# Optimization experiments

Hardware: AMD Instinct MI355X
Metric: run time of the kernel (lower is better)

## Reference

```python
import jax, jax.numpy as jnp
import numpy as np

DIM = 256
B, W_IN, H_IN = 8, 96, 96


def setup_inputs() -> dict:
    key = jax.random.key(0)
    k1, k2, k3 = jax.random.split(key, 3)
    x = jax.random.normal(k1, (B, W_IN, H_IN, DIM), dtype=jnp.float32)
    # Conv2d(dim, 3*dim, kernel_size=1): weight (3C, C) (1x1 spatial dropped), bias (3C,)
    w_qkv = jax.random.normal(k2, (3 * DIM, DIM), dtype=jnp.float32) * (1.0 / np.sqrt(DIM))
    b_qkv = jax.random.normal(k3, (3 * DIM,), dtype=jnp.float32) * 0.01
    return {"x": x, "w_qkv": w_qkv, "b_qkv": b_qkv}


def reference(x, w_qkv, b_qkv):
    # x: (B, W, H, C) -> transpose(3,1) -> (B, C, H, W)
    xt = jnp.transpose(x, (0, 3, 2, 1))
    # 1x1 conv == channel GEMM
    qvk = jnp.einsum('bchw,oc->bohw', xt, w_qkv) + b_qkv[None, :, None, None]
    q, k, v = jnp.split(qvk, 3, axis=1)  # each (B, C, H, W)
    Bn, C, H, W = q.shape

    q_t = jnp.transpose(q, (0, 2, 1, 3))            # (B, H, C, W)
    qk = q_t.reshape(Bn, H * C, W)                   # (B, H*C, W)
    qf = q_t.reshape(Bn, H, C * W)                   # (B, H, C*W)
    kq = jnp.transpose(k, (0, 1, 3, 2)).reshape(Bn, C * W, H)  # (B, C*W, H)
    ms = jax.nn.softmax(jnp.matmul(qf, kq), axis=-1)  # (B, H, H) attention over H

    kf = jnp.transpose(k, (0, 3, 2, 1)).reshape(Bn, W, H * C)  # (B, W, H*C)
    ma = jax.nn.softmax(jnp.matmul(kf, qk), axis=-1)  # (B, W, W) attention over W

    vq = jnp.transpose(v, (0, 2, 1, 3)).reshape(Bn, H, C * W)  # (B, H, C*W)
    vk = jnp.transpose(v, (0, 3, 2, 1)).reshape(Bn, W, H * C)  # (B, W, H*C)

    ms = jnp.matmul(ms, vq).reshape(Bn, H, C, W)     # view(B, H, C, W)
    ms = jnp.transpose(ms, (0, 2, 1, 3))             # (B, C, H, W)
    ma = jnp.matmul(ma, vk).reshape(Bn, W, H, C)     # view(B, W, H, C)
    ma = jnp.transpose(ma, (0, 3, 2, 1))             # (B, C, H, W)

    # final transpose(3,1): (B, C, H, W) -> (B, W, H, C)
    return jnp.transpose(ms + ma, (0, 3, 2, 1))
```

## Files before the change

kernel.cpp:

```cpp
#include <hip/hip_runtime.h>
#include <math.h>

#define SQ 96
#define CQ 256
#define HWQ 9216
#define PIXQ 73728

typedef __attribute__((ext_vector_type(8))) __bf16 bf16x8;
typedef __attribute__((ext_vector_type(4))) float f32x4;

union FragU { uint4 u; bf16x8 b; };

__device__ inline uint32_t bf16_rne_u(float f) {
  uint32_t u = __float_as_uint(f);
  return (u + 0x7FFFu + ((u >> 16) & 1u)) >> 16;
}
__device__ inline uint32_t pack_split(float f) {
  uint32_t hi = bf16_rne_u(f);
  float rem = f - __uint_as_float(hi << 16);
  uint32_t lo = __float_as_uint(rem) >> 16;
  return hi | (lo << 16);
}

__device__ inline const uint32_t* swzc(const uint32_t* base, int row, int colb) {
  return base + row * 32 + ((colb ^ ((row & 7) << 4)) >> 2);
}

__device__ inline void lds_dma16(const void* g, void* l) {
  __builtin_amdgcn_global_load_lds(
      (const __attribute__((address_space(1))) uint32_t*)g,
      (__attribute__((address_space(3))) uint32_t*)l, 16, 0, 0);
}

__device__ inline void pack8_store(float4 va, float4 vb_, int m, int kc,
                                   int k8, uint32_t* __restrict__ dst) {
  uint32_t p0 = pack_split(va.x), p1 = pack_split(va.y);
  uint32_t p2 = pack_split(va.z), p3 = pack_split(va.w);
  uint32_t p4 = pack_split(vb_.x), p5 = pack_split(vb_.y);
  uint32_t p6 = pack_split(vb_.z), p7 = pack_split(vb_.w);
  uint32_t h[4], l[4];
  h[0] = (p0 & 0xFFFFu) | (p1 << 16);
  h[1] = (p2 & 0xFFFFu) | (p3 << 16);
  h[2] = (p4 & 0xFFFFu) | (p5 << 16);
  h[3] = (p6 & 0xFFFFu) | (p7 << 16);
  l[0] = (p0 >> 16) | (p1 & 0xFFFF0000u);
  l[1] = (p2 >> 16) | (p3 & 0xFFFF0000u);
  l[2] = (p4 >> 16) | (p5 & 0xFFFF0000u);
  l[3] = (p6 >> 16) | (p7 & 0xFFFF0000u);
  int swz = (m & 7) << 4;
  uint32_t* rowp = dst + ((size_t)m * 8 + kc) * 32;
  *(uint4*)(rowp + (((k8 * 16) ^ swz) >> 2)) = *(uint4*)h;
  *(uint4*)(rowp + (((64 + k8 * 16) ^ swz) >> 2)) = *(uint4*)l;
}

__global__ __launch_bounds__(256) void prep_b_kernel(
    const float* __restrict__ w, uint32_t* __restrict__ Bps) {
  __shared__ float grow[256];
  const int blk = blockIdx.x;
  if (blk < 256) {
    const int cp = threadIdx.x;
    float acc = 0.0f;
#pragma unroll 4
    for (int o = 0; o < 256; ++o)
      acc += w[o * 256 + blk] * w[(256 + o) * 256 + cp];
    grow[cp] = acc;
    __syncthreads();
    if (threadIdx.x < 32) {
      int rem = threadIdx.x * 8;
      float4 va = *(const float4*)(grow + rem);
      float4 vb_ = *(const float4*)(grow + rem + 4);
      pack8_store(va, vb_, blk, rem >> 5, (rem & 31) >> 3, Bps);
    }
  } else {
    int r = (blk - 256) * 8 + (threadIdx.x >> 5);
    int rem = (threadIdx.x & 31) * 8;
    const float* s = w + (size_t)(512 + r) * 256 + rem;
    float4 va = *(const float4*)s;
    float4 vb_ = *(const float4*)(s + 4);
    pack8_store(va, vb_, 256 + r, rem >> 5, (rem & 31) >> 3, Bps);
  }
}

__global__ __launch_bounds__(256) void prep_vec_kernel(
    const float* __restrict__ w, const float* __restrict__ bias,
    float* __restrict__ tvec, float* __restrict__ svec) {
  const int c = threadIdx.x;
  if (blockIdx.x == 0) {
    float t = 0.0f;
#pragma unroll 4
    for (int o = 0; o < 256; ++o) t += bias[o] * w[(256 + o) * 256 + c];
    tvec[c] = t;
  } else {
    float s = 0.0f;
#pragma unroll 4
    for (int o = 0; o < 256; ++o) s += bias[256 + o] * w[o * 256 + c];
    svec[c] = s;
  }
}

__global__ __launch_bounds__(256) void split_x_kernel(
    const float* __restrict__ x, const float* __restrict__ tvec,
    const float* __restrict__ svec, uint32_t* __restrict__ xps,
    float* __restrict__ dtp, float* __restrict__ dsp) {
  int rec = blockIdx.x * 256 + threadIdx.x;
  int m = rec >> 3;
  int kc = rec & 7;
  const float* s = x + (size_t)m * 256 + kc * 32;
  const float* tv = tvec + kc * 32;
  const float* sv = svec + kc * 32;
  float dt = 0.0f, ds = 0.0f;
#pragma unroll
  for (int g = 0; g < 4; ++g) {
    float4 va = *(const float4*)(s + g * 8);
    float4 vb_ = *(const float4*)(s + g * 8 + 4);
    pack8_store(va, vb_, m, kc, g, xps);
    const float* tg = tv + g * 8;
    const float* sg = sv + g * 8;
    dt += va.x * tg[0] + va.y * tg[1] + va.z * tg[2] + va.w * tg[3]
        + vb_.x * tg[4] + vb_.y * tg[5] + vb_.z * tg[6] + vb_.w * tg[7];
    ds += va.x * sg[0] + va.y * sg[1] + va.z * sg[2] + va.w * sg[3]
        + vb_.x * sg[4] + vb_.y * sg[5] + vb_.z * sg[6] + vb_.w * sg[7];
  }
#pragma unroll
  for (int off = 1; off < 8; off <<= 1) {
    dt += __shfl_xor(dt, off);
    ds += __shfl_xor(ds, off);
  }
  if ((rec & 7) == 0) {
    dtp[m] = dt;
    dsp[m] = ds;
  }
}

__global__ __launch_bounds__(256) void reduce_ag_kernel(
    const float* __restrict__ dtp, const float* __restrict__ dsp,
    float* __restrict__ alpha, float* __restrict__ gamma) {
  const int b = blockIdx.x;
  const int t = threadIdx.x;
  if (t < 96) {
    float a = 0.0f;
#pragma unroll 4
    for (int wi = 0; wi < 96; ++wi) a += dtp[b * HWQ + wi * SQ + t];
    alpha[b * SQ + t] = a;
  } else if (t >= 128 && t < 224) {
    int wi = t - 128;
    float g = 0.0f;
#pragma unroll 4
    for (int hh = 0; hh < 96; ++hh) g += dsp[b * HWQ + wi * SQ + hh];
    gamma[b * SQ + wi] = g;
  }
}

__global__ __launch_bounds__(256) void qkv_gemm_mfma(
    const uint32_t* __restrict__ xps, const uint32_t* __restrict__ Bps,
    const float* __restrict__ bias, ushort* __restrict__ yps,
    ushort* __restrict__ vb) {
  __shared__ uint32_t Apk[128 * 32];
  __shared__ uint32_t Bpk[128 * 32];
  const int tid = threadIdx.x;
  const int lane = tid & 63;
  const int wid = tid >> 6;
  const int wm = wid >> 1, wn = wid & 1;
  const int lr = lane & 15, quad = lane >> 4;
  const int lin = (blockIdx.x & 7) * 288 + (blockIdx.x >> 3);
  const int m0 = (lin >> 2) * 128, n0 = (lin & 3) * 128;
  const int srow = tid >> 3;
  const int scol = (tid & 7) * 4;

  const uint32_t* aP = xps + (size_t)(m0 + srow) * 256 + scol;
  const uint32_t* bP = Bps + (size_t)(n0 + srow) * 256 + scol;

  f32x4 acc[4][4] = {};

  for (int kc = 0; kc < 8; ++kc) {
#pragma unroll
    for (int j = 0; j < 4; ++j) {
      lds_dma16(aP + j * 8192 + kc * 32, &Apk[j * 1024 + tid * 4]);
      lds_dma16(bP + j * 8192 + kc * 32, &Bpk[j * 1024 + tid * 4]);
    }
    __syncthreads();

    FragU ah[4], al[4], bh[4], bl[4];
#pragma unroll
    for (int t = 0; t < 4; ++t) {
      const int ra = wm * 64 + t * 16 + lr;
      ah[t].u = *(const uint4*)swzc(Apk, ra, quad * 16);
      al[t].u = *(const uint4*)swzc(Apk, ra, 64 + quad * 16);
      const int rb = wn * 64 + t * 16 + lr;
      bh[t].u = *(const uint4*)swzc(Bpk, rb, quad * 16);
      bl[t].u = *(const uint4*)swzc(Bpk, rb, 64 + quad * 16);
    }
#pragma unroll
    for (int i = 0; i < 4; ++i)
#pragma unroll
      for (int j = 0; j < 4; ++j) {
        acc[i][j] = __builtin_amdgcn_mfma_f32_16x16x32_bf16(al[i].b, bh[j].b, acc[i][j], 0, 0, 0);
        acc[i][j] = __builtin_amdgcn_mfma_f32_16x16x32_bf16(ah[i].b, bl[j].b, acc[i][j], 0, 0, 0);
        acc[i][j] = __builtin_amdgcn_mfma_f32_16x16x32_bf16(ah[i].b, bh[j].b, acc[i][j], 0, 0, 0);
      }
    __syncthreads();
  }

  if (n0 < 256) {
#pragma unroll
    for (int i = 0; i < 4; ++i) {
      const int growb = m0 + wm * 64 + i * 16 + quad * 4;
#pragma unroll
      for (int r = 0; r < 4; ++r) {
        int p = growb + r;
        size_t b16 = (size_t)p * 512;
        int sw = (p & 7) << 4;
#pragma unroll
        for (int j = 0; j < 4; ++j) {
          int o = n0 + wn * 64 + j * 16 + lr;
          int ci = o & 31, kc = o >> 5;
          uint32_t ps = pack_split(acc[i][j][r]);
          size_t rb = b16 + (size_t)kc * 64;
          yps[rb + (((ci * 2) ^ sw) >> 1)] = (ushort)ps;
          yps[rb + (((64 + ci * 2) ^ sw) >> 1)] = (ushort)(ps >> 16);
        }
      }
    }
  } else {
#pragma unroll
    for (int i = 0; i < 4; ++i) {
      const int growb = m0 + wm * 64 + i * 16 + quad * 4;
#pragma unroll
      for (int r = 0; r < 4; ++r) {
        int p = growb + r;
        int b = p / HWQ;
        int rem = p - b * HWQ;
        int ww = rem / SQ;
        int hh = rem - ww * SQ;
        size_t opix = (size_t)b * HWQ + (size_t)hh * SQ + ww;
#pragma unroll
        for (int j = 0; j < 4; ++j) {
          int o = n0 + wn * 64 + j * 16 + lr;
          float val = acc[i][j][r] + bias[256 + o];
          vb[opix * 256 + (o - 256)] = (ushort)bf16_rne_u(val);
        }
      }
    }
  }
}

__global__ __launch_bounds__(256) void attn_scores_mfma(
    const ushort* __restrict__ xf, const ushort* __restrict__ yf,
    float* __restrict__ Sp) {
  __shared__ uint32_t Xpk[96 * 32];
  __shared__ uint32_t Ypk[96 * 32];
  const int tid = threadIdx.x;
  const int lane = tid & 63;
  const int wid = tid >> 6;
  const int wm = wid >> 1, wn = wid & 1;
  const int lr = lane & 15, quad = lane >> 4;
  const int chunk = blockIdx.x;
  const int b = blockIdx.y;
  const int which = blockIdx.z;
  const ushort* Xf = which ? yf : xf;
  const ushort* Yf = which ? xf : yf;
  const int srow = tid >> 3;
  const int byteoff = (tid & 7) * 16;

  f32x4 acc[3][3] = {};

  for (int it = 0; it < 24; ++it) {
    int kout = chunk * 3 + (it >> 3);
    int kc = it & 7;
#pragma unroll
    for (int j = 0; j < 3; ++j) {
      int row = j * 32 + srow;
      int pm = which ? (row * SQ + kout) : (kout * SQ + row);
      int pix = b * HWQ + pm;
      int nom = byteoff ^ (((row & 7) ^ (pix & 7)) << 4);
      size_t off = ((size_t)pix * 8 + kc) * 64 + (nom >> 1);
      lds_dma16(Xf + off, &Xpk[j * 1024 + tid * 4]);
      lds_dma16(Yf + off, &Ypk[j * 1024 + tid * 4]);
    }
    __syncthreads();

    FragU xh[3], xl[3], yh[3], yl[3];
#pragma unroll
    for (int t = 0; t < 3; ++t) {
      const int rx = wm * 48 + t * 16 + lr;
      xh[t].u = *(const uint4*)swzc(Xpk, rx, quad * 16);
      xl[t].u = *(const uint4*)swzc(Xpk, rx, 64 + quad * 16);
      const int ry = wn * 48 + t * 16 + lr;
      yh[t].u = *(const uint4*)swzc(Ypk, ry, quad * 16);
      yl[t].u = *(const uint4*)swzc(Ypk, ry, 64 + quad * 16);
    }
#pragma unroll
    for (int i = 0; i < 3; ++i)
#pragma unroll
      for (int j = 0; j < 3; ++j) {
        acc[i][j] = __builtin_amdgcn_mfma_f32_16x16x32_bf16(xl[i].b, yh[j].b, acc[i][j], 0, 0, 0);
        acc[i][j] = __builtin_amdgcn_mfma_f32_16x16x32_bf16(xh[i].b, yl[j].b, acc[i][j], 0, 0, 0);
        acc[i][j] = __builtin_amdgcn_mfma_f32_16x16x32_bf16(xh[i].b, yh[j].b, acc[i][j], 0, 0, 0);
      }
    __syncthreads();
  }
  float* S = Sp + ((size_t)(which * 8 + b) * 32 + chunk) * (size_t)HWQ;
#pragma unroll
  for (int i = 0; i < 3; ++i)
#pragma unroll
    for (int r = 0; r < 4; ++r)
#pragma unroll
      for (int j = 0; j < 3; ++j) {
        int row = wm * 48 + i * 16 + quad * 4 + r;
        int col = wn * 48 + j * 16 + lr;
        S[(size_t)row * SQ + col] = acc[i][j][r];
      }
}

__global__ __launch_bounds__(256) void softmax_p(
    const float* __restrict__ Sp, const float* __restrict__ alpha,
    const float* __restrict__ gamma, ushort* __restrict__ Pms,
    ushort* __restrict__ Pma) {
  const int tid = threadIdx.x;
  const int lane = tid & 63;
  const int row = blockIdx.x * 4 + (tid >> 6);
  const int wsel = row >= 768;
  const int rr = row - wsel * 768;
  const int b = rr / SQ;
  const int hr = rr - b * SQ;
  const float* base = Sp + ((size_t)(wsel * 8 + b) * 32) * (size_t)HWQ
                      + (size_t)hr * SQ;
  float v0 = 0.0f, s1 = 0.0f;
#pragma unroll 4
  for (int ch = 0; ch < 32; ++ch) {
    const float* p = base + (size_t)ch * HWQ;
    v0 += p[lane];
    if (lane < 32) s1 += p[64 + lane];
  }
  const float* corr = (wsel ? gamma : alpha) + b * SQ;
  v0 += corr[lane];
  ushort* q = wsel ? (Pma + (size_t)rr * SQ) : (Pms + (size_t)rr * SQ);
  float v1 = (lane < 32) ? (s1 + corr[64 + lane]) : -3.0e38f;
  float m = fmaxf(v0, v1);
#pragma unroll
  for (int off = 32; off > 0; off >>= 1) m = fmaxf(m, __shfl_xor(m, off));
  float e0 = __expf(v0 - m);
  float e1 = (lane < 32) ? __expf(v1 - m) : 0.0f;
  float s = e0 + e1;
#pragma unroll
  for (int off = 32; off > 0; off >>= 1) s += __shfl_xor(s, off);
  float inv = 1.0f / s;
  q[lane] = (ushort)bf16_rne_u(e0 * inv);
  if (lane < 32) q[64 + lane] = (ushort)bf16_rne_u(e1 * inv);
}

__global__ __launch_bounds__(256) void attn_apply_mfma(
    const ushort* __restrict__ vb, const ushort* __restrict__ P,
    float* __restrict__ out, const int which) {
  __shared__ ushort Vt[256 * 40];
  const int tid = threadIdx.x;
  const int lane = tid & 63;
  const int wid = tid >> 6;
  const int wm = wid >> 1, wn = wid & 1;
  const int lr = lane & 15, quad = lane >> 4;
  const int xi = blockIdx.x;
  const int b = blockIdx.y;

  f32x4 acc[3][8] = {};

  for (int k0 = 0; k0 < 96; k0 += 32) {
#pragma unroll
    for (int j = 0; j < 8; ++j) {
      int bi = j * 256 + tid;
      int c2 = bi & 127;
      int k2 = bi >> 7;
      int k = k0 + k2 * 2;
      int c = c2 * 2;
      size_t r0, r1;
      if (which == 0) {
        r0 = ((size_t)b * HWQ + (size_t)k * SQ + xi) * CQ + c;
        r1 = r0 + (size_t)SQ * CQ;
      } else {
        r0 = ((size_t)b * HWQ + (size_t)xi * SQ + k) * CQ + c;
        r1 = r0 + CQ;
      }
      uint32_t a0 = *(const uint32_t*)(vb + r0);
      uint32_t a1 = *(const uint32_t*)(vb + r1);
      uint32_t w0 = (a0 & 0xFFFFu) | (a1 << 16);
      uint32_t w1 = (a0 >> 16) | (a1 & 0xFFFF0000u);
      *(uint32_t*)&Vt[c * 40 + k2 * 2] = w0;
      *(uint32_t*)&Vt[(c + 1) * 40 + k2 * 2] = w1;
    }
    __syncthreads();
    FragU a[3];
#pragma unroll
    for (int t = 0; t < 3; ++t) {
      int row = wm * 48 + t * 16 + lr;
      const ushort* ps = P + ((size_t)b * SQ + row) * SQ + k0 + quad * 8;
      a[t].u = *(const uint4*)ps;
    }
#pragma unroll
    for (int j = 0; j < 8; ++j) {
      int cb = wn * 128 + j * 16 + lr;
      FragU bf;
      bf.u = *(const uint4*)&Vt[cb * 40 + quad * 8];
#pragma unroll
      for (int i = 0; i < 3; ++i)
        acc[i][j] = __builtin_amdgcn_mfma_f32_16x16x32_bf16(a[i].b, bf.b, acc[i][j], 0, 0, 0);
    }
    __syncthreads();
  }

#pragma unroll
  for (int i = 0; i < 3; ++i) {
#pragma unroll
    for (int r = 0; r < 4; ++r) {
      int mrow = wm * 48 + i * 16 + quad * 4 + r;
      size_t obase;
      if (which == 0) obase = (((size_t)b * SQ + xi) * SQ + mrow) * CQ;
      else            obase = (((size_t)b * SQ + mrow) * SQ + xi) * CQ;
#pragma unroll
      for (int j = 0; j < 8; ++j) {
        int c = wn * 128 + j * 16 + lr;
        if (which == 0) out[obase + c] = acc[i][j][r];
        else            out[obase + c] += acc[i][j][r];
      }
    }
  }
}

extern "C" void kernel_launch(void* const* d_in, const int* in_sizes, int n_in,
                              void* d_out, int out_size, void* d_ws,
                              size_t ws_size, hipStream_t stream) {
  const float* x = (const float*)d_in[0];
  const float* w = (const float*)d_in[1];
  const float* bias = (const float*)d_in[2];
  float* out = (float*)d_out;

  ushort* yps = (ushort*)d_ws;
  ushort* vb  = yps + (size_t)PIXQ * 512;
  ushort* Pms = vb + (size_t)PIXQ * 256;
  ushort* Pma = Pms + PIXQ;
  float*  Sp  = (float*)(Pma + PIXQ);
  uint32_t* Bps = (uint32_t*)(Sp + (size_t)2 * 8 * 32 * HWQ);
  float* tvec = (float*)(Bps + 512 * 256);
  float* svec = tvec + 256;
  float* alpha = svec + 256;
  float* gamma = alpha + 768;
  float* dtp = gamma + 768;
  float* dsp = dtp + PIXQ;

  uint32_t* xps = (uint32_t*)d_out;

  prep_b_kernel<<<dim3(288), 256, 0, stream>>>(w, Bps);
  prep_vec_kernel<<<dim3(2), 256, 0, stream>>>(w, bias, tvec, svec);
  split_x_kernel<<<dim3(2304), 256, 0, stream>>>(x, tvec, svec, xps, dtp, dsp);
  reduce_ag_kernel<<<dim3(8), 256, 0, stream>>>(dtp, dsp, alpha, gamma);
  qkv_gemm_mfma<<<dim3(2304), 256, 0, stream>>>(xps, Bps, bias, yps, vb);
  attn_scores_mfma<<<dim3(32, 8, 2), 256, 0, stream>>>((const ushort*)xps, yps, Sp);
  softmax_p<<<dim3(384), 256, 0, stream>>>(Sp, alpha, gamma, Pms, Pma);
  attn_apply_mfma<<<dim3(96, 8), 256, 0, stream>>>(vb, Pms, out, 0);
  attn_apply_mfma<<<dim3(96, 8), 256, 0, stream>>>(vb, Pma, out, 1);
}
```

Before: 436.5 us.

## Store split-bf16 operands unswizzled and swizzle on load; split attn_apply channels

Packed hi/lo bf16 operands are now written to global memory in linear order, and the XOR swizzle is applied on the load side (per-thread source column in the GEMM, LDS DMA offsets in the scores kernel). This makes the packing stores contiguous, and split_x now writes whole records as grouped vector stores. attn_apply_mfma is split across two channel halves via blockIdx.z, halving its accumulator registers and LDS and doubling the grid. A XOR slot swizzle is added to its transposed V tile in LDS to reduce bank conflicts. The cost is extra index arithmetic, and the added P-matrix reloads across the two channel blocks.

```diff
diff --git a/kernel.cpp b/kernel.cpp
--- a/kernel.cpp
+++ b/kernel.cpp
@@ -32,25 +32,26 @@
       (__attribute__((address_space(3))) uint32_t*)l, 16, 0, 0);
 }
 
-__device__ inline void pack8_store(float4 va, float4 vb_, int m, int kc,
-                                   int k8, uint32_t* __restrict__ dst) {
+__device__ inline void split8(float4 va, float4 vb_, uint4& h, uint4& l) {
   uint32_t p0 = pack_split(va.x), p1 = pack_split(va.y);
   uint32_t p2 = pack_split(va.z), p3 = pack_split(va.w);
   uint32_t p4 = pack_split(vb_.x), p5 = pack_split(vb_.y);
   uint32_t p6 = pack_split(vb_.z), p7 = pack_split(vb_.w);
-  uint32_t h[4], l[4];
-  h[0] = (p0 & 0xFFFFu) | (p1 << 16);
-  h[1] = (p2 & 0xFFFFu) | (p3 << 16);
-  h[2] = (p4 & 0xFFFFu) | (p5 << 16);
-  h[3] = (p6 & 0xFFFFu) | (p7 << 16);
-  l[0] = (p0 >> 16) | (p1 & 0xFFFF0000u);
-  l[1] = (p2 >> 16) | (p3 & 0xFFFF0000u);
-  l[2] = (p4 >> 16) | (p5 & 0xFFFF0000u);
-  l[3] = (p6 >> 16) | (p7 & 0xFFFF0000u);
-  int swz = (m & 7) << 4;
-  uint32_t* rowp = dst + ((size_t)m * 8 + kc) * 32;
-  *(uint4*)(rowp + (((k8 * 16) ^ swz) >> 2)) = *(uint4*)h;
-  *(uint4*)(rowp + (((64 + k8 * 16) ^ swz) >> 2)) = *(uint4*)l;
+  h.x = (p0 & 0xFFFFu) | (p1 << 16);
+  h.y = (p2 & 0xFFFFu) | (p3 << 16);
+  h.z = (p4 & 0xFFFFu) | (p5 << 16);
+  h.w = (p6 & 0xFFFFu) | (p7 << 16);
+  l.x = (p0 >> 16) | (p1 & 0xFFFF0000u);
+  l.y = (p2 >> 16) | (p3 & 0xFFFF0000u);
+  l.z = (p4 >> 16) | (p5 & 0xFFFF0000u);
+  l.w = (p6 >> 16) | (p7 & 0xFFFF0000u);
+}
+
+__device__ inline void store_g8(uint32_t* __restrict__ dst, int rec, int k8,
+                                uint4 h, uint4 l) {
+  uint32_t* rowp = dst + (size_t)rec * 32;
+  *(uint4*)(rowp + k8 * 4) = h;
+  *(uint4*)(rowp + 16 + k8 * 4) = l;
 }
 
 __global__ __launch_bounds__(256) void prep_b_kernel(
@@ -67,17 +68,17 @@
     __syncthreads();
     if (threadIdx.x < 32) {
       int rem = threadIdx.x * 8;
-      float4 va = *(const float4*)(grow + rem);
-      float4 vb_ = *(const float4*)(grow + rem + 4);
-      pack8_store(va, vb_, blk, rem >> 5, (rem & 31) >> 3, Bps);
+      uint4 h, l;
+      split8(*(const float4*)(grow + rem), *(const float4*)(grow + rem + 4), h, l);
+      store_g8(Bps, blk * 8 + (rem >> 5), (rem & 31) >> 3, h, l);
     }
   } else {
     int r = (blk - 256) * 8 + (threadIdx.x >> 5);
     int rem = (threadIdx.x & 31) * 8;
     const float* s = w + (size_t)(512 + r) * 256 + rem;
-    float4 va = *(const float4*)s;
-    float4 vb_ = *(const float4*)(s + 4);
-    pack8_store(va, vb_, 256 + r, rem >> 5, (rem & 31) >> 3, Bps);
+    uint4 h, l;
+    split8(*(const float4*)s, *(const float4*)(s + 4), h, l);
+    store_g8(Bps, (256 + r) * 8 + (rem >> 5), (rem & 31) >> 3, h, l);
   }
 }
 
@@ -108,12 +109,13 @@
   const float* s = x + (size_t)m * 256 + kc * 32;
   const float* tv = tvec + kc * 32;
   const float* sv = svec + kc * 32;
+  uint4 hh[4], ll[4];
   float dt = 0.0f, ds = 0.0f;
 #pragma unroll
   for (int g = 0; g < 4; ++g) {
     float4 va = *(const float4*)(s + g * 8);
     float4 vb_ = *(const float4*)(s + g * 8 + 4);
-    pack8_store(va, vb_, m, kc, g, xps);
+    split8(va, vb_, hh[g], ll[g]);
     const float* tg = tv + g * 8;
     const float* sg = sv + g * 8;
     dt += va.x * tg[0] + va.y * tg[1] + va.z * tg[2] + va.w * tg[3]
@@ -121,6 +123,11 @@
     ds += va.x * sg[0] + va.y * sg[1] + va.z * sg[2] + va.w * sg[3]
         + vb_.x * sg[4] + vb_.y * sg[5] + vb_.z * sg[6] + vb_.w * sg[7];
   }
+  uint32_t* rowp = xps + (size_t)rec * 32;
+#pragma unroll
+  for (int g = 0; g < 4; ++g) *(uint4*)(rowp + g * 4) = hh[g];
+#pragma unroll
+  for (int g = 0; g < 4; ++g) *(uint4*)(rowp + 16 + g * 4) = ll[g];
 #pragma unroll
   for (int off = 1; off < 8; off <<= 1) {
     dt += __shfl_xor(dt, off);
@@ -165,10 +172,10 @@
   const int lin = (blockIdx.x & 7) * 288 + (blockIdx.x >> 3);
   const int m0 = (lin >> 2) * 128, n0 = (lin & 3) * 128;
   const int srow = tid >> 3;
-  const int scol = (tid & 7) * 4;
-
-  const uint32_t* aP = xps + (size_t)(m0 + srow) * 256 + scol;
-  const uint32_t* bP = Bps + (size_t)(n0 + srow) * 256 + scol;
+  const int sg = ((tid & 7) ^ (srow & 7)) * 4;
+
+  const uint32_t* aP = xps + (size_t)(m0 + srow) * 256 + sg;
+  const uint32_t* bP = Bps + (size_t)(n0 + srow) * 256 + sg;
 
   f32x4 acc[4][4] = {};
 
@@ -209,15 +216,14 @@
       for (int r = 0; r < 4; ++r) {
         int p = growb + r;
         size_t b16 = (size_t)p * 512;
-        int sw = (p & 7) << 4;
 #pragma unroll
         for (int j = 0; j < 4; ++j) {
           int o = n0 + wn * 64 + j * 16 + lr;
           int ci = o & 31, kc = o >> 5;
           uint32_t ps = pack_split(acc[i][j][r]);
           size_t rb = b16 + (size_t)kc * 64;
-          yps[rb + (((ci * 2) ^ sw) >> 1)] = (ushort)ps;
-          yps[rb + (((64 + ci * 2) ^ sw) >> 1)] = (ushort)(ps >> 16);
+          yps[rb + ci] = (ushort)ps;
+          yps[rb + 32 + ci] = (ushort)(ps >> 16);
         }
       }
     }
@@ -272,8 +278,8 @@
       int row = j * 32 + srow;
       int pm = which ? (row * SQ + kout) : (kout * SQ + row);
       int pix = b * HWQ + pm;
-      int nom = byteoff ^ (((row & 7) ^ (pix & 7)) << 4);
-      size_t off = ((size_t)pix * 8 + kc) * 64 + (nom >> 1);
+      int nom = byteoff ^ ((row & 7) << 4);
+      size_t off = (size_t)pix * 512 + kc * 64 + (nom >> 1);
       lds_dma16(Xf + off, &Xpk[j * 1024 + tid * 4]);
       lds_dma16(Yf + off, &Ypk[j * 1024 + tid * 4]);
     }
@@ -352,7 +358,7 @@
 __global__ __launch_bounds__(256) void attn_apply_mfma(
     const ushort* __restrict__ vb, const ushort* __restrict__ P,
     float* __restrict__ out, const int which) {
-  __shared__ ushort Vt[256 * 40];
+  __shared__ ushort Vt[128 * 40];
   const int tid = threadIdx.x;
   const int lane = tid & 63;
   const int wid = tid >> 6;
@@ -360,17 +366,18 @@
   const int lr = lane & 15, quad = lane >> 4;
   const int xi = blockIdx.x;
   const int b = blockIdx.y;
-
-  f32x4 acc[3][8] = {};
+  const int ch = blockIdx.z;
+
+  f32x4 acc[3][4] = {};
 
   for (int k0 = 0; k0 < 96; k0 += 32) {
 #pragma unroll
-    for (int j = 0; j < 8; ++j) {
+    for (int j = 0; j < 4; ++j) {
       int bi = j * 256 + tid;
-      int c2 = bi & 127;
-      int k2 = bi >> 7;
+      int c2 = bi & 63;
+      int k2 = bi >> 6;
       int k = k0 + k2 * 2;
-      int c = c2 * 2;
+      int c = ch * 128 + c2 * 2;
       size_t r0, r1;
       if (which == 0) {
         r0 = ((size_t)b * HWQ + (size_t)k * SQ + xi) * CQ + c;
@@ -383,22 +390,24 @@
       uint32_t a1 = *(const uint32_t*)(vb + r1);
       uint32_t w0 = (a0 & 0xFFFFu) | (a1 << 16);
       uint32_t w1 = (a0 >> 16) | (a1 & 0xFFFF0000u);
-      *(uint32_t*)&Vt[c * 40 + k2 * 2] = w0;
-      *(uint32_t*)&Vt[(c + 1) * 40 + k2 * 2] = w1;
+      int cl = c2 * 2;
+      int slot = k2 ^ (c2 & 12);
+      *(uint32_t*)&Vt[cl * 40 + slot * 2] = w0;
+      *(uint32_t*)&Vt[(cl + 1) * 40 + slot * 2] = w1;
     }
     __syncthreads();
     FragU a[3];
 #pragma unroll
     for (int t = 0; t < 3; ++t) {
       int row = wm * 48 + t * 16 + lr;
-      const ushort* ps = P + ((size_t)b * SQ + row) * SQ + k0 + quad * 8;
-      a[t].u = *(const uint4*)ps;
-    }
-#pragma unroll
-    for (int j = 0; j < 8; ++j) {
-      int cb = wn * 128 + j * 16 + lr;
+      a[t].u = *(const uint4*)(P + ((size_t)b * SQ + row) * SQ + k0 + quad * 8);
+    }
+#pragma unroll
+    for (int j = 0; j < 4; ++j) {
+      int cb = wn * 64 + j * 16 + lr;
+      int slot = (quad * 4) ^ ((cb >> 1) & 12);
       FragU bf;
-      bf.u = *(const uint4*)&Vt[cb * 40 + quad * 8];
+      bf.u = *(const uint4*)&Vt[cb * 40 + slot * 2];
 #pragma unroll
       for (int i = 0; i < 3; ++i)
         acc[i][j] = __builtin_amdgcn_mfma_f32_16x16x32_bf16(a[i].b, bf.b, acc[i][j], 0, 0, 0);
@@ -407,21 +416,19 @@
   }
 
 #pragma unroll
-  for (int i = 0; i < 3; ++i) {
+  for (int i = 0; i < 3; ++i)
 #pragma unroll
     for (int r = 0; r < 4; ++r) {
       int mrow = wm * 48 + i * 16 + quad * 4 + r;
-      size_t obase;
-      if (which == 0) obase = (((size_t)b * SQ + xi) * SQ + mrow) * CQ;
-      else            obase = (((size_t)b * SQ + mrow) * SQ + xi) * CQ;
-#pragma unroll
-      for (int j = 0; j < 8; ++j) {
-        int c = wn * 128 + j * 16 + lr;
+      size_t obase = which ? (((size_t)b * SQ + mrow) * SQ + xi) * CQ
+                           : (((size_t)b * SQ + xi) * SQ + mrow) * CQ;
+#pragma unroll
+      for (int j = 0; j < 4; ++j) {
+        int c = ch * 128 + wn * 64 + j * 16 + lr;
         if (which == 0) out[obase + c] = acc[i][j][r];
         else            out[obase + c] += acc[i][j][r];
       }
     }
-  }
 }
 
 extern "C" void kernel_launch(void* const* d_in, const int* in_sizes, int n_in,
@@ -454,6 +461,6 @@
   qkv_gemm_mfma<<<dim3(2304), 256, 0, stream>>>(xps, Bps, bias, yps, vb);
   attn_scores_mfma<<<dim3(32, 8, 2), 256, 0, stream>>>((const ushort*)xps, yps, Sp);
   softmax_p<<<dim3(384), 256, 0, stream>>>(Sp, alpha, gamma, Pms, Pma);
-  attn_apply_mfma<<<dim3(96, 8), 256, 0, stream>>>(vb, Pms, out, 0);
-  attn_apply_mfma<<<dim3(96, 8), 256, 0, stream>>>(vb, Pma, out, 1);
-}
+  attn_apply_mfma<<<dim3(96, 8, 2), 256, 0, stream>>>(vb, Pms, out, 0);
+  attn_apply_mfma<<<dim3(96, 8, 2), 256, 0, stream>>>(vb, Pma, out, 1);
+}
```

New measurement: 391.7 us. 10.3% less time.
